# Performance work log

Hardware: AMD Instinct MI355X
Metric: run time of the kernel (lower is better)

## Reference

```python
import jax, jax.numpy as jnp
import numpy as np

ANCHORS = np.array([[116., 90.], [156., 198.], [373., 326.],
                    [30., 61.], [62., 45.], [59., 119.],
                    [10., 13.], [16., 30.], [33., 23.]], dtype=np.float32)
IMG_WH = (416.0, 416.0)  # image_size[::-1]
IGNORE_THRESH = 0.5
MAX_BOXES = 64  # static upper bound on true boxes per image per layer


def bce_logits(t, x):
    # tf.nn.sigmoid_cross_entropy_with_logits(labels=t, logits=x)
    return jnp.maximum(x, 0.0) - x * t + jnp.log1p(jnp.exp(-jnp.abs(x)))


def box_iou(b1, b2):
    # b1: [B,H,W,3,4] xywh, b2: [B,M,4] xywh -> iou [B,H,W,3,M]
    b1 = b1[..., None, :]
    b2 = b2[:, None, None, None, :, :]
    b1_min = b1[..., :2] - b1[..., 2:4] * 0.5
    b1_max = b1[..., :2] + b1[..., 2:4] * 0.5
    b2_min = b2[..., :2] - b2[..., 2:4] * 0.5
    b2_max = b2[..., :2] + b2[..., 2:4] * 0.5
    inter_wh = jnp.maximum(jnp.minimum(b1_max, b2_max) - jnp.maximum(b1_min, b2_min), 0.0)
    inter = inter_wh[..., 0] * inter_wh[..., 1]
    a1 = b1[..., 2] * b1[..., 3]
    a2 = b2[..., 2] * b2[..., 3]
    return inter / (a1 + a2 - inter)


def layer_loss(yt, pred, anchors):
    # yt: [B,H,W,3,5+C], pred: [B,H,W,3*(5+C)]
    B, H, W = yt.shape[:3]
    C = pred.shape[-1] // 3 - 5
    p = pred.reshape(B, H, W, 3, 5 + C)
    gy, gx = jnp.meshgrid(jnp.arange(H), jnp.arange(W), indexing='ij')
    grid = jnp.stack([gx, gy], -1).astype(pred.dtype)[:, :, None, :]  # [H,W,1,2]
    fwh = jnp.array([W, H], pred.dtype)
    anc = anchors.reshape(1, 1, 1, 3, 2)
    # pred_process (channel layout: 0=conf, 1:3=xy, 3:5=wh, 5:=class)
    xy = (jax.nn.sigmoid(p[..., 1:3]) + grid) / fwh
    wh = jnp.exp(p[..., 3:5]) * anc / fwh
    conf = jax.nn.sigmoid(p[..., 0:1])
    cls = jax.nn.sigmoid(p[..., 5:])
    pred_box = jnp.concatenate([xy, wh], -1)

    obj = yt[..., 0:1]
    true_cls = yt[..., 5:]
    true_xy = yt[..., 1:3] * fwh - grid
    true_wh = jnp.log(yt[..., 3:5] / anc * jnp.array(IMG_WH, yt.dtype))
    true_wh = jnp.where(obj > 0, true_wh, jnp.zeros_like(true_wh))
    scale = 2.0 - yt[..., 3:4] * yt[..., 4:5]

    # vectorized replacement for the per-image while_loop + boolean_mask:
    # gather the MAX_BOXES highest-objectness cells per image as candidate true boxes
    flat_obj = obj[..., 0].reshape(B, -1)
    flat_box = yt[..., 1:5].reshape(B, -1, 4)
    vals, idx = jax.lax.top_k(flat_obj, MAX_BOXES)
    tboxes = jnp.take_along_axis(flat_box, idx[..., None], axis=1)  # [B,M,4]
    iou = box_iou(pred_box, tboxes)                                 # [B,H,W,3,M]
    iou = jnp.where((vals > 0.5)[:, None, None, None, :], iou, -jnp.inf)
    best_iou = jnp.max(iou, axis=-1)  # -inf when no true boxes (matches tf reduce_max over empty)
    ignore = (best_iou < IGNORE_THRESH).astype(yt.dtype)[..., None]

    xy_l = obj * scale * bce_logits(true_xy, xy)
    wh_l = obj * scale * 0.5 * jnp.square(true_wh - wh)
    conf_l = obj * bce_logits(obj, conf) + (1.0 - obj) * bce_logits(obj, conf) * ignore
    cls_l = obj * bce_logits(true_cls, cls)
    red = lambda t: jnp.sum(t, axis=(1, 2, 3, 4))
    return red(xy_l) + red(wh_l) + red(conf_l) + red(cls_l)


def yolo_loss(y_true, p0, p1, p2):
    B, _, A, D = y_true.shape
    yts = [y_true[:, 0:169].reshape(B, 13, 13, A, D),
           y_true[:, 169:845].reshape(B, 26, 26, A, D),
           y_true[:, 845:3549].reshape(B, 52, 52, A, D)]
    anc = jnp.asarray(ANCHORS)
    total = jnp.zeros((B,), y_true.dtype)
    for i, pred in enumerate([p0, p1, p2]):
        total = total + layer_loss(yts[i], pred, anc[3 * i:3 * i + 3])
    return total


def setup_inputs() -> dict:
    key = jax.random.key(0)
    B, N, C = 32, 3549, 80
    k1, k2, k3, k4, k5, k6, k7 = jax.random.split(key, 7)
    obj = (jax.random.uniform(k1, (B, N, 3, 1)) < 0.002).astype(jnp.float32)
    xy = jax.random.uniform(k2, (B, N, 3, 2), minval=0.05, maxval=0.95)
    wh = jax.random.uniform(k3, (B, N, 3, 2), minval=0.05, maxval=0.4)
    cls = (jax.random.uniform(k4, (B, N, 3, C)) < (1.0 / C)).astype(jnp.float32)
    y_true = jnp.concatenate([obj, xy, wh, cls], axis=-1)
    pred_13 = 0.5 * jax.random.normal(k5, (B, 13, 13, 255), dtype=jnp.float32)
    pred_26 = 0.5 * jax.random.normal(k6, (B, 26, 26, 255), dtype=jnp.float32)
    pred_52 = 0.5 * jax.random.normal(k7, (B, 52, 52, 255), dtype=jnp.float32)
    return {"y_true": y_true, "pred_13": pred_13, "pred_26": pred_26, "pred_52": pred_52}


def reference(y_true, pred_13, pred_26, pred_52):
    return yolo_loss(y_true, pred_13, pred_26, pred_52)
```

## Files before the change

kernel.cpp:

```cpp
#include <hip/hip_runtime.h>

#define NPAIR 96
#define MAXB 64
#define CAP 256

__constant__ float c_anc[9][2] = {
    {116.f, 90.f}, {156.f, 198.f}, {373.f, 326.f},
    { 30.f, 61.f}, { 62.f, 45.f}, { 59.f, 119.f},
    { 10.f, 13.f}, { 16.f, 30.f}, { 33.f, 23.f}};

__device__ __forceinline__ float sigm(float x) { return 1.f / (1.f + expf(-x)); }

__device__ __forceinline__ float bce_f(float t, float x) {
    return fmaxf(x, 0.f) - x * t + logf(1.f + expf(-fabsf(x)));
}

__device__ __forceinline__ void map_block(int j, int& l, int& blk, int& S, int& n0) {
    if (j < 2)       { l = 0; blk = j;      S = 13; n0 = 0;   }
    else if (j < 10) { l = 1; blk = j - 2;  S = 26; n0 = 169; }
    else             { l = 2; blk = j - 10; S = 52; n0 = 845; }
}

__global__ __launch_bounds__(256) void scan_k(
    const float* __restrict__ yt, unsigned long long* __restrict__ bmp_all,
    float* __restrict__ out)
{
    int bid = blockIdx.x;
    int tid = threadIdx.x;
    if (bid == 0 && tid < 32) out[tid] = 0.f;
    int b = bid / 42;
    int j = bid - b * 42;
    int l, blk, S, n0;
    map_block(j, l, blk, S, n0);
    int nCells = S * S * 3;
    int c = blk * 256 + tid;
    const float* ybase = yt + (long long)(b * 3549 + n0) * 255;
    float ov = (c < nCells) ? ybase[(long long)c * 85] : 0.f;
    unsigned long long m = __ballot(ov > 0.5f);
    if ((tid & 63) == 0)
        bmp_all[(long long)(b * 3 + l) * 128 + (c >> 6)] = m;
}

__global__ __launch_bounds__(256) void pos_k(
    const float* __restrict__ yt,
    const float* __restrict__ p13, const float* __restrict__ p26,
    const float* __restrict__ p52,
    float4* __restrict__ oboxes, int* __restrict__ counts,
    const unsigned long long* __restrict__ bmp_all,
    float* __restrict__ out)
{
    int pair = blockIdx.x;
    int b = pair / 3;
    int l = pair - b * 3;
    int S  = (l == 0) ? 13 : (l == 1) ? 26 : 52;
    int n0 = (l == 0) ? 0  : (l == 1) ? 169 : 845;
    int nwords = (l == 0) ? 8 : (l == 1) ? 32 : 128;
    float Sf = (float)S;
    const float* ybase = yt + (long long)(b * 3549 + n0) * 255;
    const float* pred  = (l == 0) ? p13 : (l == 1) ? p26 : p52;
    const float* pbase = pred + (long long)b * S * S * 255;
    const unsigned long long* bmp = bmp_all + (long long)pair * 128;

    __shared__ int spc[128];
    __shared__ int sidx[CAP];
    __shared__ int stot;

    int tid = threadIdx.x;
    unsigned long long w = 0ULL;
    if (tid < 128) {
        w = (tid < nwords) ? bmp[tid] : 0ULL;
        spc[tid] = __popcll(w);
    }
    __syncthreads();
    if (tid < 128) {
        int base = 0;
        for (int jj = 0; jj < tid; ++jj) base += spc[jj];
        unsigned long long ww = w;
        while (ww) {
            int bit = __ffsll((long long)ww) - 1;
            if (base < CAP) sidx[base] = tid * 64 + bit;
            ++base;
            ww &= ww - 1;
        }
        if (tid == 127) stot = base;
    }
    __syncthreads();

    int TC = stot < CAP ? stot : CAP;
    int MB = TC < MAXB ? TC : MAXB;
    if (tid == 0) counts[pair] = MB;
    if (tid < MB) {
        int idx = sidx[tid];
        const float* yc = ybase + (long long)idx * 85;
        oboxes[pair * MAXB + tid] = make_float4(yc[1], yc[2], yc[3], yc[4]);
    }

    int wv = tid >> 6, lane = tid & 63;
    float wsum = 0.f;
    for (int i = wv; i < TC; i += 4) {
        int idx = sidx[i];
        const float* yc = ybase + (long long)idx * 85;
        const float* pc = pbase + (long long)idx * 85;
        float part = bce_f(yc[5 + lane], sigm(pc[5 + lane]));
        if (lane < 16)
            part += bce_f(yc[69 + lane], sigm(pc[69 + lane]));
        if (lane == 0) {
            int p_ = idx / 3, a = idx - p_ * 3;
            int gh = p_ / S, gw = p_ - gh * S;
            float aw = c_anc[l * 3 + a][0], ah = c_anc[l * 3 + a][1];
            float v0 = pc[0], v1 = pc[1], v2 = pc[2], v3 = pc[3], v4 = pc[4];
            float t1 = yc[1], t2 = yc[2], t3 = yc[3], t4 = yc[4];
            part += bce_f(1.f, sigm(v0));
            float sc = 2.f - t3 * t4;
            float px = (sigm(v1) + (float)gw) / Sf;
            float py = (sigm(v2) + (float)gh) / Sf;
            part += sc * (bce_f(t1 * Sf - (float)gw, px) +
                          bce_f(t2 * Sf - (float)gh, py));
            float pw = expf(v3) * aw / Sf, ph = expf(v4) * ah / Sf;
            float twx = logf(t3 / aw * 416.f), twy = logf(t4 / ah * 416.f);
            part += sc * 0.5f * ((twx - pw) * (twx - pw) + (twy - ph) * (twy - ph));
        }
        for (int off = 32; off > 0; off >>= 1)
            part += __shfl_down(part, off, 64);
        if (lane == 0) wsum += part;
    }
    if (lane == 0) atomicAdd(out + b, wsum);
}

__global__ __launch_bounds__(256) void neg_k(
    const float* __restrict__ p13, const float* __restrict__ p26,
    const float* __restrict__ p52,
    const float4* __restrict__ oboxes, const int* __restrict__ counts,
    const unsigned long long* __restrict__ bmp_all,
    float* __restrict__ out)
{
    int bid = blockIdx.x;
    int tid = threadIdx.x;
    int b = bid / 42;
    int j = bid - b * 42;
    int l, blk, S, n0;
    map_block(j, l, blk, S, n0);
    (void)n0;
    int nCells = S * S * 3;
    int pair = b * 3 + l;
    float Sf = (float)S;
    const float* pred  = (l == 0) ? p13 : (l == 1) ? p26 : p52;
    const float* pbase = pred + (long long)b * S * S * 255;

    __shared__ float sxmin[MAXB], sxmax[MAXB], symin[MAXB], symax[MAXB], sba[MAXB];
    int count = counts[pair];
    if (tid < count) {
        float4 g = oboxes[pair * MAXB + tid];
        sxmin[tid] = g.x - g.z * 0.5f;
        sxmax[tid] = g.x + g.z * 0.5f;
        symin[tid] = g.y - g.w * 0.5f;
        symax[tid] = g.y + g.w * 0.5f;
        sba[tid]   = g.z * g.w;
    }
    __syncthreads();

    float loss = 0.f;
    int c = blk * 256 + tid;
    if (c < nCells) {
        unsigned long long word = bmp_all[(long long)pair * 128 + (c >> 6)];
        if (!((word >> (c & 63)) & 1ULL)) {
            const float* pc = pbase + (long long)c * 85;
            float v0 = pc[0];
            if (count == 0) {
                loss = bce_f(0.f, sigm(v0));
            } else {
                float v1 = pc[1], v2 = pc[2], v3 = pc[3], v4 = pc[4];
                int p_ = c / 3, a = c - p_ * 3;
                int gh = p_ / S, gw = p_ - gh * S;
                float aw = c_anc[l * 3 + a][0], ah = c_anc[l * 3 + a][1];
                float px = (sigm(v1) + (float)gw) / Sf;
                float py = (sigm(v2) + (float)gh) / Sf;
                float pw = expf(v3) * aw / Sf, ph = expf(v4) * ah / Sf;
                float pxmin = px - pw * 0.5f, pxmax = px + pw * 0.5f;
                float pymin = py - ph * 0.5f, pymax = py + ph * 0.5f;
                float parea = pw * ph;
                bool hit = false;
#pragma unroll 4
                for (int i = 0; i < count; ++i) {
                    float iw = fminf(pxmax, sxmax[i]) - fmaxf(pxmin, sxmin[i]);
                    float ih = fminf(pymax, symax[i]) - fmaxf(pymin, symin[i]);
                    float inter = fmaxf(iw, 0.f) * fmaxf(ih, 0.f);
                    hit = hit || (3.f * inter >= parea + sba[i]);
                }
                if (!hit) loss = bce_f(0.f, sigm(v0));
            }
        }
    }

    for (int off = 32; off > 0; off >>= 1)
        loss += __shfl_down(loss, off, 64);
    __shared__ float wsum[4];
    if ((tid & 63) == 0) wsum[tid >> 6] = loss;
    __syncthreads();
    if (tid == 0)
        atomicAdd(out + b, wsum[0] + wsum[1] + wsum[2] + wsum[3]);
}

extern "C" void kernel_launch(void* const* d_in, const int* in_sizes, int n_in,
                              void* d_out, int out_size, void* d_ws, size_t ws_size,
                              hipStream_t stream) {
    (void)in_sizes; (void)n_in; (void)out_size; (void)ws_size;
    const float* yt  = (const float*)d_in[0];
    const float* p13 = (const float*)d_in[1];
    const float* p26 = (const float*)d_in[2];
    const float* p52 = (const float*)d_in[3];
    float* out = (float*)d_out;

    unsigned long long* bmp = (unsigned long long*)d_ws;
    float4* oboxes = (float4*)((char*)d_ws + NPAIR * 128 * 8);
    int* counts    = (int*)((char*)d_ws + NPAIR * 128 * 8 + NPAIR * MAXB * 16);

    scan_k<<<32 * 42, 256, 0, stream>>>(yt, bmp, out);
    pos_k<<<NPAIR, 256, 0, stream>>>(yt, p13, p26, p52, oboxes, counts, bmp, out);
    neg_k<<<32 * 42, 256, 0, stream>>>(p13, p26, p52, oboxes, counts, bmp, out);
}
```

Baseline: 245.2 us.

## Fuse objectness scan into positive-loss kernel and replace serial prefix sum

Merges the scan kernel into the per-(image,layer) positive kernel, so each of the 96 blocks scans its own objectness column into shared memory, removing one kernel launch and a global bitmap round trip. The serial popcount prefix loop becomes a wavefront shuffle scan. Positive-loss partials go to a workspace array that the negative kernel adds in, which drops the per-wave atomics. The negative kernel also loads the first four prediction channels as one vector. The risk is that only 96 blocks now do the whole strided yt scan (up to 32 loads per thread on the largest layer), which may serialize on memory latency.

```diff
diff --git a/kernel.cpp b/kernel.cpp
--- a/kernel.cpp
+++ b/kernel.cpp
@@ -9,72 +9,91 @@
     { 30.f, 61.f}, { 62.f, 45.f}, { 59.f, 119.f},
     { 10.f, 13.f}, { 16.f, 30.f}, { 33.f, 23.f}};
 
+typedef float floatx4 __attribute__((ext_vector_type(4), aligned(4)));
+
 __device__ __forceinline__ float sigm(float x) { return 1.f / (1.f + expf(-x)); }
 
 __device__ __forceinline__ float bce_f(float t, float x) {
     return fmaxf(x, 0.f) - x * t + logf(1.f + expf(-fabsf(x)));
 }
 
-__device__ __forceinline__ void map_block(int j, int& l, int& blk, int& S, int& n0) {
-    if (j < 2)       { l = 0; blk = j;      S = 13; n0 = 0;   }
-    else if (j < 10) { l = 1; blk = j - 2;  S = 26; n0 = 169; }
-    else             { l = 2; blk = j - 10; S = 52; n0 = 845; }
-}
-
-__global__ __launch_bounds__(256) void scan_k(
-    const float* __restrict__ yt, unsigned long long* __restrict__ bmp_all,
-    float* __restrict__ out)
-{
-    int bid = blockIdx.x;
-    int tid = threadIdx.x;
-    if (bid == 0 && tid < 32) out[tid] = 0.f;
-    int b = bid / 42;
-    int j = bid - b * 42;
-    int l, blk, S, n0;
-    map_block(j, l, blk, S, n0);
-    int nCells = S * S * 3;
-    int c = blk * 256 + tid;
-    const float* ybase = yt + (long long)(b * 3549 + n0) * 255;
-    float ov = (c < nCells) ? ybase[(long long)c * 85] : 0.f;
-    unsigned long long m = __ballot(ov > 0.5f);
-    if ((tid & 63) == 0)
-        bmp_all[(long long)(b * 3 + l) * 128 + (c >> 6)] = m;
-}
-
-__global__ __launch_bounds__(256) void pos_k(
+__device__ __forceinline__ void map_block(int j, int& l, int& blk, int& S) {
+    if (j < 2)       { l = 0; blk = j;      S = 13; }
+    else if (j < 10) { l = 1; blk = j - 2;  S = 26; }
+    else             { l = 2; blk = j - 10; S = 52; }
+}
+
+template <int ITERS>
+__device__ __forceinline__ void scan_obj(const float* __restrict__ ybase,
+                                         int nCells, int tid,
+                                         unsigned long long* swords) {
+    float ov[ITERS];
+#pragma unroll
+    for (int k = 0; k < ITERS; ++k) {
+        int c = tid + (k << 8);
+        ov[k] = (c < nCells) ? ybase[(long long)c * 85] : 0.f;
+    }
+    int lane = tid & 63, wv = tid >> 6;
+#pragma unroll
+    for (int k = 0; k < ITERS; ++k) {
+        unsigned long long m = __ballot(ov[k] > 0.5f);
+        if (lane == 0) swords[k * 4 + wv] = m;
+    }
+}
+
+__global__ __launch_bounds__(256) void prep_k(
     const float* __restrict__ yt,
     const float* __restrict__ p13, const float* __restrict__ p26,
     const float* __restrict__ p52,
     float4* __restrict__ oboxes, int* __restrict__ counts,
-    const unsigned long long* __restrict__ bmp_all,
-    float* __restrict__ out)
+    unsigned long long* __restrict__ bmp_all,
+    float* __restrict__ posloss, float* __restrict__ out)
 {
     int pair = blockIdx.x;
+    int tid = threadIdx.x;
     int b = pair / 3;
     int l = pair - b * 3;
-    int S  = (l == 0) ? 13 : (l == 1) ? 26 : 52;
-    int n0 = (l == 0) ? 0  : (l == 1) ? 169 : 845;
-    int nwords = (l == 0) ? 8 : (l == 1) ? 32 : 128;
+    int S      = (l == 0) ? 13  : (l == 1) ? 26  : 52;
+    int n0     = (l == 0) ? 0   : (l == 1) ? 169 : 845;
+    int nwords = (l == 0) ? 8   : (l == 1) ? 32  : 128;
+    int nCells = S * S * 3;
     float Sf = (float)S;
     const float* ybase = yt + (long long)(b * 3549 + n0) * 255;
     const float* pred  = (l == 0) ? p13 : (l == 1) ? p26 : p52;
     const float* pbase = pred + (long long)b * S * S * 255;
-    const unsigned long long* bmp = bmp_all + (long long)pair * 128;
-
-    __shared__ int spc[128];
+
+    if (pair == 0 && tid < 32) out[tid] = 0.f;
+
+    __shared__ unsigned long long swords[128];
     __shared__ int sidx[CAP];
-    __shared__ int stot;
-
-    int tid = threadIdx.x;
+    __shared__ int sbase[2];
+    __shared__ int stot_s;
+    __shared__ float pls[4];
+
+    if (l == 0)      scan_obj<2 >(ybase, nCells, tid, swords);
+    else if (l == 1) scan_obj<8 >(ybase, nCells, tid, swords);
+    else             scan_obj<32>(ybase, nCells, tid, swords);
+    __syncthreads();
+
+    int lane = tid & 63, wv = tid >> 6;
     unsigned long long w = 0ULL;
+    int pc = 0;
     if (tid < 128) {
-        w = (tid < nwords) ? bmp[tid] : 0ULL;
-        spc[tid] = __popcll(w);
-    }
-    __syncthreads();
+        w = (tid < nwords) ? swords[tid] : 0ULL;
+        pc = __popcll(w);
+    }
+    int x = pc;
+#pragma unroll
+    for (int d = 1; d < 64; d <<= 1) {
+        int y = __shfl_up(x, d, 64);
+        if (lane >= d) x += y;
+    }
+    if (tid < 128 && lane == 63) sbase[wv] = x;
+    if (tid < nwords) bmp_all[(long long)pair * 128 + tid] = w;
+    __syncthreads();
+    if (tid == 0) stot_s = sbase[0] + sbase[1];
     if (tid < 128) {
-        int base = 0;
-        for (int jj = 0; jj < tid; ++jj) base += spc[jj];
+        int base = x - pc + (wv ? sbase[0] : 0);
         unsigned long long ww = w;
         while (ww) {
             int bit = __ffsll((long long)ww) - 1;
@@ -82,10 +101,10 @@
             ++base;
             ww &= ww - 1;
         }
-        if (tid == 127) stot = base;
-    }
-    __syncthreads();
-
+    }
+    __syncthreads();
+
+    int stot = stot_s;
     int TC = stot < CAP ? stot : CAP;
     int MB = TC < MAXB ? TC : MAXB;
     if (tid == 0) counts[pair] = MB;
@@ -95,20 +114,19 @@
         oboxes[pair * MAXB + tid] = make_float4(yc[1], yc[2], yc[3], yc[4]);
     }
 
-    int wv = tid >> 6, lane = tid & 63;
     float wsum = 0.f;
     for (int i = wv; i < TC; i += 4) {
         int idx = sidx[i];
         const float* yc = ybase + (long long)idx * 85;
-        const float* pc = pbase + (long long)idx * 85;
-        float part = bce_f(yc[5 + lane], sigm(pc[5 + lane]));
+        const float* pc_ = pbase + (long long)idx * 85;
+        float part = bce_f(yc[5 + lane], sigm(pc_[5 + lane]));
         if (lane < 16)
-            part += bce_f(yc[69 + lane], sigm(pc[69 + lane]));
+            part += bce_f(yc[69 + lane], sigm(pc_[69 + lane]));
         if (lane == 0) {
             int p_ = idx / 3, a = idx - p_ * 3;
             int gh = p_ / S, gw = p_ - gh * S;
             float aw = c_anc[l * 3 + a][0], ah = c_anc[l * 3 + a][1];
-            float v0 = pc[0], v1 = pc[1], v2 = pc[2], v3 = pc[3], v4 = pc[4];
+            float v0 = pc_[0], v1 = pc_[1], v2 = pc_[2], v3 = pc_[3], v4 = pc_[4];
             float t1 = yc[1], t2 = yc[2], t3 = yc[3], t4 = yc[4];
             part += bce_f(1.f, sigm(v0));
             float sc = 2.f - t3 * t4;
@@ -120,11 +138,14 @@
             float twx = logf(t3 / aw * 416.f), twy = logf(t4 / ah * 416.f);
             part += sc * 0.5f * ((twx - pw) * (twx - pw) + (twy - ph) * (twy - ph));
         }
+#pragma unroll
         for (int off = 32; off > 0; off >>= 1)
             part += __shfl_down(part, off, 64);
         if (lane == 0) wsum += part;
     }
-    if (lane == 0) atomicAdd(out + b, wsum);
+    if (lane == 0) pls[wv] = wsum;
+    __syncthreads();
+    if (tid == 0) posloss[pair] = pls[0] + pls[1] + pls[2] + pls[3];
 }
 
 __global__ __launch_bounds__(256) void neg_k(
@@ -132,15 +153,14 @@
     const float* __restrict__ p52,
     const float4* __restrict__ oboxes, const int* __restrict__ counts,
     const unsigned long long* __restrict__ bmp_all,
-    float* __restrict__ out)
+    const float* __restrict__ posloss, float* __restrict__ out)
 {
     int bid = blockIdx.x;
     int tid = threadIdx.x;
     int b = bid / 42;
     int j = bid - b * 42;
-    int l, blk, S, n0;
-    map_block(j, l, blk, S, n0);
-    (void)n0;
+    int l, blk, S;
+    map_block(j, l, blk, S);
     int nCells = S * S * 3;
     int pair = b * 3 + l;
     float Sf = (float)S;
@@ -165,17 +185,18 @@
         unsigned long long word = bmp_all[(long long)pair * 128 + (c >> 6)];
         if (!((word >> (c & 63)) & 1ULL)) {
             const float* pc = pbase + (long long)c * 85;
-            float v0 = pc[0];
+            floatx4 v03 = *(const floatx4*)pc;
+            float v0 = v03.x;
             if (count == 0) {
                 loss = bce_f(0.f, sigm(v0));
             } else {
-                float v1 = pc[1], v2 = pc[2], v3 = pc[3], v4 = pc[4];
+                float v4 = pc[4];
                 int p_ = c / 3, a = c - p_ * 3;
                 int gh = p_ / S, gw = p_ - gh * S;
                 float aw = c_anc[l * 3 + a][0], ah = c_anc[l * 3 + a][1];
-                float px = (sigm(v1) + (float)gw) / Sf;
-                float py = (sigm(v2) + (float)gh) / Sf;
-                float pw = expf(v3) * aw / Sf, ph = expf(v4) * ah / Sf;
+                float px = (sigm(v03.y) + (float)gw) / Sf;
+                float py = (sigm(v03.z) + (float)gh) / Sf;
+                float pw = expf(v03.w) * aw / Sf, ph = expf(v4) * ah / Sf;
                 float pxmin = px - pw * 0.5f, pxmax = px + pw * 0.5f;
                 float pymin = py - ph * 0.5f, pymax = py + ph * 0.5f;
                 float parea = pw * ph;
@@ -191,7 +212,9 @@
             }
         }
     }
-
+    if (tid == 0 && blk == 0) loss += posloss[pair];
+
+#pragma unroll
     for (int off = 32; off > 0; off >>= 1)
         loss += __shfl_down(loss, off, 64);
     __shared__ float wsum[4];
@@ -214,8 +237,11 @@
     unsigned long long* bmp = (unsigned long long*)d_ws;
     float4* oboxes = (float4*)((char*)d_ws + NPAIR * 128 * 8);
     int* counts    = (int*)((char*)d_ws + NPAIR * 128 * 8 + NPAIR * MAXB * 16);
-
-    scan_k<<<32 * 42, 256, 0, stream>>>(yt, bmp, out);
-    pos_k<<<NPAIR, 256, 0, stream>>>(yt, p13, p26, p52, oboxes, counts, bmp, out);
-    neg_k<<<32 * 42, 256, 0, stream>>>(p13, p26, p52, oboxes, counts, bmp, out);
-}
+    float* posloss = (float*)((char*)d_ws + NPAIR * 128 * 8 + NPAIR * MAXB * 16
+                              + NPAIR * sizeof(int));
+
+    prep_k<<<NPAIR, 256, 0, stream>>>(yt, p13, p26, p52, oboxes, counts, bmp,
+                                      posloss, out);
+    neg_k<<<32 * 42, 256, 0, stream>>>(p13, p26, p52, oboxes, counts, bmp,
+                                       posloss, out);
+}
```

New measurement: 259.8 us. 1.06x slower.
